# Kernel optimization log

Measured on AMD Instinct MI355X. Metric: run time of the kernel, lower is better.

## Reference

```python
import jax, jax.numpy as jnp
import numpy as np

S, B, C, H = 2048, 2, 512, 8
CC = C // H


def setup_inputs() -> dict:
    key = jax.random.key(0)
    ks = jax.random.split(key, 8)
    x = jax.random.normal(ks[0], (S, B, C), dtype=jnp.float32)
    pe = jax.random.normal(ks[1], (S, B, C), dtype=jnp.float32)
    # strict causal mask: True means masked-out (future positions t > s)
    idx = jnp.arange(S)
    content_mask = (idx[None, :] > idx[:, None])  # (s, t)
    content_mask = jnp.broadcast_to(content_mask[:, :, None], (S, S, B))
    pad = jnp.full((B,), S, dtype=jnp.int64)  # full-length sequences (unused in training path)
    scale = 0.02
    Wqkv = jax.random.normal(ks[2], (3 * C, C), dtype=jnp.float32) * scale
    bqkv = jax.random.normal(ks[3], (3 * C,), dtype=jnp.float32) * scale
    Wc = jax.random.normal(ks[4], (C, C), dtype=jnp.float32) * scale
    bc = jax.random.normal(ks[5], (C,), dtype=jnp.float32) * scale
    return {"x": x, "pe": pe, "content_mask": content_mask, "pad": pad,
            "Wqkv": Wqkv, "bqkv": bqkv, "Wc": Wc, "bc": bc}


def reference(x, pe, content_mask, pad, Wqkv, bqkv, Wc, bc):
    s, b, c = x.shape
    h, cc = H, CC
    qkv = jnp.einsum('sbc,dc->sbd', x + pe, Wqkv) + bqkv  # (s, b, 3c)
    q, k, v = jnp.split(qkv, 3, axis=-1)
    q = q.reshape(s, b, h, cc)
    k = k.reshape(s, b, h, cc)
    v = v.reshape(s, b, h, cc)
    temperature = 1.0 / np.sqrt(cc).astype(np.float32)
    qk = jnp.einsum('sbhc,tbhc->stbh', q, k) * temperature  # (s, t, b, h)
    a = jnp.where(content_mask[:, :, :, None], -jnp.inf, qk)
    p = jax.nn.softmax(a, axis=1)  # softmax over t (dim=1), matching torch
    out = jnp.einsum('stbh,tbhc->sbhc', p, v).reshape(s, b, c)
    out = jnp.einsum('sbc,dc->sbd', out, Wc) + bc
    return out
```

## Files before the change

kernel.cpp:

```cpp
#include <hip/hip_runtime.h>
#include <hip/hip_bf16.h>

#define S_LEN 2048
#define BATCH 2
#define CDIM  512
#define HEADS 8
#define HDIM  64
#define QKVD  1536

typedef float          f32x4  __attribute__((ext_vector_type(4)));
typedef __bf16         bf16x8 __attribute__((ext_vector_type(8)));
typedef unsigned short u16x8  __attribute__((ext_vector_type(8)));

typedef __attribute__((address_space(1))) const unsigned int* gas_ptr;
typedef __attribute__((address_space(3))) unsigned int* las_ptr;

static __device__ __forceinline__ unsigned short f2bf(float x) {
  union { float f; unsigned u; } v; v.f = x;
  unsigned r = v.u + 0x7fffu + ((v.u >> 16) & 1u);
  return (unsigned short)(r >> 16);
}

__global__ void __launch_bounds__(256) prep_kernel(
    const float* __restrict__ x, const float* __restrict__ pe,
    const float* __restrict__ wqkv, const float* __restrict__ wc,
    unsigned short* __restrict__ xpe_bf,
    unsigned short* __restrict__ wqkv_bf,
    unsigned short* __restrict__ wc_bf) {
  const int N1 = S_LEN * BATCH * CDIM;
  const int N2 = QKVD * CDIM;
  const int NP = (N1 + N2 + CDIM * CDIM) / 8;
  const int pkt = blockIdx.x * 256 + threadIdx.x;
  if (pkt >= NP) return;
  int i = pkt * 8;
  u16x8 o;
  if (i < N1) {
    f32x4 a0 = *reinterpret_cast<const f32x4*>(x + i);
    f32x4 a1 = *reinterpret_cast<const f32x4*>(x + i + 4);
    f32x4 b0 = *reinterpret_cast<const f32x4*>(pe + i);
    f32x4 b1 = *reinterpret_cast<const f32x4*>(pe + i + 4);
#pragma unroll
    for (int j = 0; j < 4; ++j) { o[j] = f2bf(a0[j] + b0[j]); o[4 + j] = f2bf(a1[j] + b1[j]); }
    *reinterpret_cast<u16x8*>(xpe_bf + i) = o;
  } else if (i < N1 + N2) {
    i -= N1;
    f32x4 a0 = *reinterpret_cast<const f32x4*>(wqkv + i);
    f32x4 a1 = *reinterpret_cast<const f32x4*>(wqkv + i + 4);
#pragma unroll
    for (int j = 0; j < 4; ++j) { o[j] = f2bf(a0[j]); o[4 + j] = f2bf(a1[j]); }
    *reinterpret_cast<u16x8*>(wqkv_bf + i) = o;
  } else {
    i -= N1 + N2;
    f32x4 a0 = *reinterpret_cast<const f32x4*>(wc + i);
    f32x4 a1 = *reinterpret_cast<const f32x4*>(wc + i + 4);
#pragma unroll
    for (int j = 0; j < 4; ++j) { o[j] = f2bf(a0[j]); o[4 + j] = f2bf(a1[j]); }
    *reinterpret_cast<u16x8*>(wc_bf + i) = o;
  }
}

template <int BM, int BN, int OUT_BF16>
__global__ void __launch_bounds__(256) gemm_lds_kernel(
    const unsigned short* __restrict__ A,
    const unsigned short* __restrict__ Bt,
    const float* __restrict__ bias,
    void* __restrict__ Cout, int M, int N, int K) {
  constexpr int FM = BM / 32;
  constexpr int FN = BN / 32;
  __shared__ unsigned short Alds[BM * 64];
  __shared__ unsigned short Blds[BN * 64];

  const int tid  = threadIdx.x;
  const int w    = tid >> 6;
  const int lane = tid & 63;
  const int wr   = w >> 1, wc = w & 1;
  const int lr   = lane & 15, hi = lane >> 4;
  const int m0   = blockIdx.y * BM;
  const int n0   = blockIdx.x * BN;

  f32x4 acc[FM][FN];
#pragma unroll
  for (int fm = 0; fm < FM; ++fm)
#pragma unroll
    for (int fn = 0; fn < FN; ++fn) acc[fm][fn] = (f32x4){0.f, 0.f, 0.f, 0.f};

  for (int kc = 0; kc < K; kc += 64) {
    __syncthreads();
#pragma unroll
    for (int i = 0; i < BM / 32; ++i) {
      const int idx = tid + i * 256;
      const int row = idx >> 3, col = (idx & 7) * 8;
      const int scol = col ^ ((row & 7) * 8);
      __builtin_amdgcn_global_load_lds(
          (gas_ptr)(const void*)(A + (size_t)(m0 + row) * K + kc + scol),
          (las_ptr)(void*)(Alds + idx * 8), 16, 0, 0);
    }
#pragma unroll
    for (int i = 0; i < BN / 32; ++i) {
      const int idx = tid + i * 256;
      const int row = idx >> 3, col = (idx & 7) * 8;
      const int scol = col ^ ((row & 7) * 8);
      __builtin_amdgcn_global_load_lds(
          (gas_ptr)(const void*)(Bt + (size_t)(n0 + row) * K + kc + scol),
          (las_ptr)(void*)(Blds + idx * 8), 16, 0, 0);
    }
    __syncthreads();

    bf16x8 af[2][FM], bfr[2][FN];
#pragma unroll
    for (int ks = 0; ks < 2; ++ks) {
#pragma unroll
      for (int fm = 0; fm < FM; ++fm) {
        const int row = wr * (BM / 2) + fm * 16 + lr;
        af[ks][fm] = *reinterpret_cast<const bf16x8*>(
            &Alds[row * 64 + ((ks * 32 + hi * 8) ^ ((row & 7) * 8))]);
      }
#pragma unroll
      for (int fn = 0; fn < FN; ++fn) {
        const int row = wc * (BN / 2) + fn * 16 + lr;
        bfr[ks][fn] = *reinterpret_cast<const bf16x8*>(
            &Blds[row * 64 + ((ks * 32 + hi * 8) ^ ((row & 7) * 8))]);
      }
    }
#pragma unroll
    for (int ks = 0; ks < 2; ++ks)
#pragma unroll
      for (int fm = 0; fm < FM; ++fm)
#pragma unroll
        for (int fn = 0; fn < FN; ++fn)
          acc[fm][fn] = __builtin_amdgcn_mfma_f32_16x16x32_bf16(
              af[ks][fm], bfr[ks][fn], acc[fm][fn], 0, 0, 0);
  }

#pragma unroll
  for (int fn = 0; fn < FN; ++fn) {
    const int n = n0 + wc * (BN / 2) + fn * 16 + lr;
    const float bv = bias[n];
#pragma unroll
    for (int fm = 0; fm < FM; ++fm) {
#pragma unroll
      for (int r = 0; r < 4; ++r) {
        const int m = m0 + wr * (BM / 2) + fm * 16 + hi * 4 + r;
        const float val = acc[fm][fn][r] + bv;
        if (OUT_BF16)
          ((unsigned short*)Cout)[(size_t)m * N + n] = f2bf(val);
        else
          ((float*)Cout)[(size_t)m * N + n] = val;
      }
    }
  }
}

#define SCALE_LOG2E 0.18033688011112042f

__device__ __forceinline__ void tile_compute(
    const bf16x8* aq, const bf16x8 kf[4][2], const bf16x8 vf[2][4],
    f32x4* acc, float* rs, unsigned short* Pw,
    int q0, int t0, int lr, int hi) {
  const f32x4 z = (f32x4){0.f, 0.f, 0.f, 0.f};
  f32x4 d[4];
#pragma unroll
  for (int ks = 0; ks < 4; ++ks) {
    f32x4 dd = __builtin_amdgcn_mfma_f32_16x16x32_bf16(aq[0], kf[ks][0], z, 0, 0, 0);
    dd = __builtin_amdgcn_mfma_f32_16x16x32_bf16(aq[1], kf[ks][1], dd, 0, 0, 0);
    d[ks] = dd;
  }
#pragma unroll
  for (int ks = 0; ks < 4; ++ks) {
    const int t = t0 + ks * 16 + lr;
#pragma unroll
    for (int rr = 0; rr < 4; ++rr) {
      const int srow = q0 + hi * 4 + rr;
      float pv = __builtin_exp2f(d[ks][rr] * SCALE_LOG2E);
      pv = (t > srow) ? 0.f : pv;
      d[ks][rr] = pv;
      rs[rr] += pv;
    }
  }
#pragma unroll
  for (int ks = 0; ks < 4; ++ks)
#pragma unroll
    for (int rr = 0; rr < 4; ++rr) {
      const int row = hi * 4 + rr;
      Pw[(row * 64 + ks * 16 + lr) ^ ((row & 7) << 3)] = f2bf(d[ks][rr]);
    }
  bf16x8 pa[2];
#pragma unroll
  for (int kk = 0; kk < 2; ++kk)
    pa[kk] = *reinterpret_cast<const bf16x8*>(
        &Pw[(lr * 64 + kk * 32 + hi * 8) ^ ((lr & 7) << 3)]);
#pragma unroll
  for (int nt = 0; nt < 4; ++nt) {
    acc[nt] = __builtin_amdgcn_mfma_f32_16x16x32_bf16(pa[0], vf[0][nt], acc[nt], 0, 0, 0);
    acc[nt] = __builtin_amdgcn_mfma_f32_16x16x32_bf16(pa[1], vf[1][nt], acc[nt], 0, 0, 0);
  }
}

__global__ void __launch_bounds__(128) attn_kernel(
    const unsigned short* __restrict__ qkv,
    unsigned short* __restrict__ attn_out) {
  __shared__ unsigned short Klds[64 * 64];
  __shared__ unsigned short Vlds[64 * 64];
  __shared__ unsigned short Plds[2][16 * 64];

  const int qb   = blockIdx.x;
  const int h    = blockIdx.y;
  const int b    = blockIdx.z;
  const int tid  = threadIdx.x;
  const int w    = tid >> 6;
  const int lane = tid & 63;
  const int lr   = lane & 15;
  const int hi   = lane >> 4;

  const int p   = qb * 2 + w;
  const int q0A = p * 16;
  const int q0B = (127 - p) * 16;
  const int NT  = ((2047 - 32 * qb) >> 6) + 1;

  const int RS = BATCH * QKVD;
  const unsigned short* Qbase = qkv + (size_t)b * QKVD + h * HDIM;
  const unsigned short* Kbase = Qbase + CDIM;
  const unsigned short* Vbase = Qbase + 2 * CDIM;

  bf16x8 aqA[2], aqB[2];
#pragma unroll
  for (int kk = 0; kk < 2; ++kk) {
    aqA[kk] = *reinterpret_cast<const bf16x8*>(
        Qbase + (size_t)(q0A + lr) * RS + kk * 32 + hi * 8);
    aqB[kk] = *reinterpret_cast<const bf16x8*>(
        Qbase + (size_t)(q0B + lr) * RS + kk * 32 + hi * 8);
  }

  f32x4 accA[4], accB[4];
  float rsA[4], rsB[4];
#pragma unroll
  for (int nt = 0; nt < 4; ++nt) {
    accA[nt] = (f32x4){0.f, 0.f, 0.f, 0.f};
    accB[nt] = (f32x4){0.f, 0.f, 0.f, 0.f};
  }
#pragma unroll
  for (int rr = 0; rr < 4; ++rr) { rsA[rr] = 0.f; rsB[rr] = 0.f; }

  const int kr = tid & 63, khalf = tid >> 6;
  const int va = tid & 31, vq = tid >> 5;
  unsigned short* Pw = Plds[w];

  for (int it = 0; it < NT; ++it) {
    const int t0 = it * 64;
    __syncthreads();
#pragma unroll
    for (int c = 0; c < 4; ++c) {
      const int cc = khalf * 4 + c;
      bf16x8 kv = *reinterpret_cast<const bf16x8*>(
          Kbase + (size_t)(t0 + kr) * RS + cc * 8);
      *reinterpret_cast<bf16x8*>(
          &Klds[(kr * 64 + cc * 8) ^ ((kr & 7) << 3)]) = kv;
    }
#pragma unroll
    for (int c = 0; c < 2; ++c) {
      const int cc = vq * 2 + c;
      const unsigned short* vp = Vbase + (size_t)(t0 + 2 * va) * RS + cc * 8;
      u16x8 v0 = *reinterpret_cast<const u16x8*>(vp);
      u16x8 v1 = *reinterpret_cast<const u16x8*>(vp + RS);
#pragma unroll
      for (int j = 0; j < 8; ++j) {
        const int dim = cc * 8 + j;
        const unsigned val = (unsigned)v0[j] | ((unsigned)v1[j] << 16);
        *reinterpret_cast<unsigned*>(
            &Vlds[(dim * 64 + 2 * va) ^ ((dim & 7) << 3)]) = val;
      }
    }
    __syncthreads();

    bf16x8 kf[4][2], vf[2][4];
#pragma unroll
    for (int ks = 0; ks < 4; ++ks)
#pragma unroll
      for (int kk = 0; kk < 2; ++kk) {
        const int row = ks * 16 + lr;
        kf[ks][kk] = *reinterpret_cast<const bf16x8*>(
            &Klds[(row * 64 + kk * 32 + hi * 8) ^ ((row & 7) << 3)]);
      }
#pragma unroll
    for (int kk = 0; kk < 2; ++kk)
#pragma unroll
      for (int nt = 0; nt < 4; ++nt) {
        const int row = nt * 16 + lr;
        vf[kk][nt] = *reinterpret_cast<const bf16x8*>(
            &Vlds[(row * 64 + kk * 32 + hi * 8) ^ ((row & 7) << 3)]);
      }

    if (t0 <= q0A + 15)
      tile_compute(aqA, kf, vf, accA, rsA, Pw, q0A, t0, lr, hi);
    if (t0 <= q0B + 15)
      tile_compute(aqB, kf, vf, accB, rsB, Pw, q0B, t0, lr, hi);
  }

#pragma unroll
  for (int rr = 0; rr < 4; ++rr) {
    float v = rsA[rr];
    v += __shfl_xor(v, 1); v += __shfl_xor(v, 2);
    v += __shfl_xor(v, 4); v += __shfl_xor(v, 8);
    rsA[rr] = 1.f / v;
    v = rsB[rr];
    v += __shfl_xor(v, 1); v += __shfl_xor(v, 2);
    v += __shfl_xor(v, 4); v += __shfl_xor(v, 8);
    rsB[rr] = 1.f / v;
  }
#pragma unroll
  for (int nt = 0; nt < 4; ++nt)
#pragma unroll
    for (int rr = 0; rr < 4; ++rr) {
      const int c = h * HDIM + nt * 16 + lr;
      const int sA = q0A + hi * 4 + rr;
      attn_out[((size_t)sA * BATCH + b) * CDIM + c] = f2bf(accA[nt][rr] * rsA[rr]);
      const int sB = q0B + hi * 4 + rr;
      attn_out[((size_t)sB * BATCH + b) * CDIM + c] = f2bf(accB[nt][rr] * rsB[rr]);
    }
}

extern "C" void kernel_launch(void* const* d_in, const int* in_sizes, int n_in,
                              void* d_out, int out_size, void* d_ws, size_t ws_size,
                              hipStream_t stream) {
  const float* x    = (const float*)d_in[0];
  const float* pe   = (const float*)d_in[1];
  const float* wqkv = (const float*)d_in[4];
  const float* bqkv = (const float*)d_in[5];
  const float* wc   = (const float*)d_in[6];
  const float* bc   = (const float*)d_in[7];

  unsigned short* xpe_bf  = (unsigned short*)d_ws;
  unsigned short* wqkv_bf = xpe_bf  + (size_t)S_LEN * BATCH * CDIM;
  unsigned short* wc_bf   = wqkv_bf + (size_t)QKVD * CDIM;
  unsigned short* qkv_bf  = wc_bf   + (size_t)CDIM * CDIM;
  unsigned short* attn_bf = qkv_bf  + (size_t)S_LEN * BATCH * QKVD;

  const int NP = (S_LEN * BATCH * CDIM + QKVD * CDIM + CDIM * CDIM) / 8;
  prep_kernel<<<dim3((NP + 255) / 256), dim3(256), 0, stream>>>(
      x, pe, wqkv, wc, xpe_bf, wqkv_bf, wc_bf);
  gemm_lds_kernel<64, 128, 1>
      <<<dim3(QKVD / 128, (S_LEN * BATCH) / 64), dim3(256), 0, stream>>>(
          xpe_bf, wqkv_bf, bqkv, (void*)qkv_bf, S_LEN * BATCH, QKVD, CDIM);
  attn_kernel<<<dim3(32, HEADS, BATCH), dim3(128), 0, stream>>>(qkv_bf, attn_bf);
  gemm_lds_kernel<64, 64, 0>
      <<<dim3(CDIM / 64, (S_LEN * BATCH) / 64), dim3(256), 0, stream>>>(
          attn_bf, wc_bf, bc, d_out, S_LEN * BATCH, CDIM, CDIM);
}
```

Before: 183.3 us.

## Write V transposed from QKV GEMM and stream K/V fragments directly in attention

The QKV GEMM epilogue now writes Q/K into a compact buffer and V transposed per (batch, head) into a separate buffer. The attention kernel drops LDS staging and barriers for K/V and loads MFMA fragments straight from global memory, double-buffered in registers. It also switches to one 16-row query tile per wave with 4 waves per block. Load balance changes: each wave handles one causal tile instead of a paired short/long pair, so work across blocks is uneven. The transposed V stores are scattered 2-byte writes, and K/V reuse across waves now depends on cache instead of LDS.

```diff
diff --git a/kernel.cpp b/kernel.cpp
--- a/kernel.cpp
+++ b/kernel.cpp
@@ -59,12 +59,13 @@
   }
 }
 
-template <int BM, int BN, int OUT_BF16>
+template <int BM, int BN, int MODE>
 __global__ void __launch_bounds__(256) gemm_lds_kernel(
     const unsigned short* __restrict__ A,
     const unsigned short* __restrict__ Bt,
     const float* __restrict__ bias,
-    void* __restrict__ Cout, int M, int N, int K) {
+    void* __restrict__ out0, unsigned short* __restrict__ out1,
+    int M, int N, int K) {
   constexpr int FM = BM / 32;
   constexpr int FN = BN / 32;
   __shared__ unsigned short Alds[BM * 64];
@@ -142,10 +143,17 @@
       for (int r = 0; r < 4; ++r) {
         const int m = m0 + wr * (BM / 2) + fm * 16 + hi * 4 + r;
         const float val = acc[fm][fn][r] + bv;
-        if (OUT_BF16)
-          ((unsigned short*)Cout)[(size_t)m * N + n] = f2bf(val);
-        else
-          ((float*)Cout)[(size_t)m * N + n] = val;
+        if (MODE == 0) {
+          ((float*)out0)[(size_t)m * N + n] = val;
+        } else {
+          if (n0 < 2 * CDIM) {
+            ((unsigned short*)out0)[(size_t)m * (2 * CDIM) + n] = f2bf(val);
+          } else {
+            const int d = n - 2 * CDIM, hh = d >> 6, dim = d & 63;
+            const int s = m >> 1, bb = m & 1;
+            out1[(((size_t)(bb * HEADS + hh)) * HDIM + dim) * S_LEN + s] = f2bf(val);
+          }
+        }
       }
     }
   }
@@ -196,126 +204,87 @@
   }
 }
 
-__global__ void __launch_bounds__(128) attn_kernel(
-    const unsigned short* __restrict__ qkv,
+#define LOADK(dst, t0)                                                      \
+  _Pragma("unroll") for (int ks = 0; ks < 4; ++ks)                          \
+  _Pragma("unroll") for (int kk = 0; kk < 2; ++kk)                          \
+    dst[ks][kk] = *reinterpret_cast<const bf16x8*>(                         \
+        Kb + (size_t)((t0) + ks * 16 + lr) * 2048 + kk * 32 + hi * 8);
+
+#define LOADV(dst, t0)                                                      \
+  _Pragma("unroll") for (int kk = 0; kk < 2; ++kk)                          \
+  _Pragma("unroll") for (int nt = 0; nt < 4; ++nt)                          \
+    dst[kk][nt] = *reinterpret_cast<const bf16x8*>(                         \
+        Vb + (size_t)(nt * 16 + lr) * 2048 + (t0) + kk * 32 + hi * 8);
+
+__global__ void __launch_bounds__(256, 2) attn_kernel(
+    const unsigned short* __restrict__ qk,
+    const unsigned short* __restrict__ vT,
     unsigned short* __restrict__ attn_out) {
-  __shared__ unsigned short Klds[64 * 64];
-  __shared__ unsigned short Vlds[64 * 64];
-  __shared__ unsigned short Plds[2][16 * 64];
-
-  const int qb   = blockIdx.x;
-  const int h    = blockIdx.y;
-  const int b    = blockIdx.z;
+  __shared__ unsigned short Plds[4][2][16 * 64];
   const int tid  = threadIdx.x;
   const int w    = tid >> 6;
   const int lane = tid & 63;
   const int lr   = lane & 15;
   const int hi   = lane >> 4;
-
-  const int p   = qb * 2 + w;
-  const int q0A = p * 16;
-  const int q0B = (127 - p) * 16;
-  const int NT  = ((2047 - 32 * qb) >> 6) + 1;
-
-  const int RS = BATCH * QKVD;
-  const unsigned short* Qbase = qkv + (size_t)b * QKVD + h * HDIM;
-  const unsigned short* Kbase = Qbase + CDIM;
-  const unsigned short* Vbase = Qbase + 2 * CDIM;
-
-  bf16x8 aqA[2], aqB[2];
-#pragma unroll
-  for (int kk = 0; kk < 2; ++kk) {
-    aqA[kk] = *reinterpret_cast<const bf16x8*>(
-        Qbase + (size_t)(q0A + lr) * RS + kk * 32 + hi * 8);
-    aqB[kk] = *reinterpret_cast<const bf16x8*>(
-        Qbase + (size_t)(q0B + lr) * RS + kk * 32 + hi * 8);
-  }
-
-  f32x4 accA[4], accB[4];
-  float rsA[4], rsB[4];
-#pragma unroll
-  for (int nt = 0; nt < 4; ++nt) {
-    accA[nt] = (f32x4){0.f, 0.f, 0.f, 0.f};
-    accB[nt] = (f32x4){0.f, 0.f, 0.f, 0.f};
-  }
-#pragma unroll
-  for (int rr = 0; rr < 4; ++rr) { rsA[rr] = 0.f; rsB[rr] = 0.f; }
-
-  const int kr = tid & 63, khalf = tid >> 6;
-  const int va = tid & 31, vq = tid >> 5;
-  unsigned short* Pw = Plds[w];
-
-  for (int it = 0; it < NT; ++it) {
-    const int t0 = it * 64;
-    __syncthreads();
-#pragma unroll
-    for (int c = 0; c < 4; ++c) {
-      const int cc = khalf * 4 + c;
-      bf16x8 kv = *reinterpret_cast<const bf16x8*>(
-          Kbase + (size_t)(t0 + kr) * RS + cc * 8);
-      *reinterpret_cast<bf16x8*>(
-          &Klds[(kr * 64 + cc * 8) ^ ((kr & 7) << 3)]) = kv;
-    }
-#pragma unroll
-    for (int c = 0; c < 2; ++c) {
-      const int cc = vq * 2 + c;
-      const unsigned short* vp = Vbase + (size_t)(t0 + 2 * va) * RS + cc * 8;
-      u16x8 v0 = *reinterpret_cast<const u16x8*>(vp);
-      u16x8 v1 = *reinterpret_cast<const u16x8*>(vp + RS);
-#pragma unroll
-      for (int j = 0; j < 8; ++j) {
-        const int dim = cc * 8 + j;
-        const unsigned val = (unsigned)v0[j] | ((unsigned)v1[j] << 16);
-        *reinterpret_cast<unsigned*>(
-            &Vlds[(dim * 64 + 2 * va) ^ ((dim & 7) << 3)]) = val;
-      }
-    }
-    __syncthreads();
-
-    bf16x8 kf[4][2], vf[2][4];
-#pragma unroll
-    for (int ks = 0; ks < 4; ++ks)
-#pragma unroll
-      for (int kk = 0; kk < 2; ++kk) {
-        const int row = ks * 16 + lr;
-        kf[ks][kk] = *reinterpret_cast<const bf16x8*>(
-            &Klds[(row * 64 + kk * 32 + hi * 8) ^ ((row & 7) << 3)]);
-      }
-#pragma unroll
-    for (int kk = 0; kk < 2; ++kk)
-#pragma unroll
-      for (int nt = 0; nt < 4; ++nt) {
-        const int row = nt * 16 + lr;
-        vf[kk][nt] = *reinterpret_cast<const bf16x8*>(
-            &Vlds[(row * 64 + kk * 32 + hi * 8) ^ ((row & 7) << 3)]);
-      }
-
-    if (t0 <= q0A + 15)
-      tile_compute(aqA, kf, vf, accA, rsA, Pw, q0A, t0, lr, hi);
-    if (t0 <= q0B + 15)
-      tile_compute(aqB, kf, vf, accB, rsB, Pw, q0B, t0, lr, hi);
-  }
+  const int h    = blockIdx.y;
+  const int b    = blockIdx.z;
+  const int qt   = 127 - (blockIdx.x * 4 + w);
+  const int q0   = qt * 16;
+  const int NT   = (q0 + 15) / 64 + 1;
+
+  const unsigned short* Qb = qk + (size_t)b * 1024 + h * HDIM;
+  const unsigned short* Kb = Qb + CDIM;
+  const unsigned short* Vb = vT + ((size_t)(b * HEADS + h)) * HDIM * S_LEN;
+
+  bf16x8 aq[2];
+#pragma unroll
+  for (int kk = 0; kk < 2; ++kk)
+    aq[kk] = *reinterpret_cast<const bf16x8*>(
+        Qb + (size_t)(q0 + lr) * 2048 + kk * 32 + hi * 8);
+
+  f32x4 acc[4];
+  float rs[4];
+#pragma unroll
+  for (int nt = 0; nt < 4; ++nt) acc[nt] = (f32x4){0.f, 0.f, 0.f, 0.f};
+#pragma unroll
+  for (int rr = 0; rr < 4; ++rr) rs[rr] = 0.f;
+
+  unsigned short* PwA = &Plds[w][0][0];
+  unsigned short* PwB = &Plds[w][1][0];
+
+  bf16x8 kfA[4][2], vfA[2][4], kfB[4][2], vfB[2][4];
+  LOADK(kfA, 0)
+  LOADV(vfA, 0)
+
+  int it = 0;
+  while (it + 1 < NT) {
+    const int tB = (it + 1) * 64;
+    LOADK(kfB, tB)
+    LOADV(vfB, tB)
+    tile_compute(aq, kfA, vfA, acc, rs, PwA, q0, it * 64, lr, hi);
+    const int tA = (it + 2 < NT) ? (it + 2) * 64 : tB;
+    LOADK(kfA, tA)
+    LOADV(vfA, tA)
+    tile_compute(aq, kfB, vfB, acc, rs, PwB, q0, tB, lr, hi);
+    it += 2;
+  }
+  if (it < NT)
+    tile_compute(aq, kfA, vfA, acc, rs, PwA, q0, it * 64, lr, hi);
 
 #pragma unroll
   for (int rr = 0; rr < 4; ++rr) {
-    float v = rsA[rr];
+    float v = rs[rr];
     v += __shfl_xor(v, 1); v += __shfl_xor(v, 2);
     v += __shfl_xor(v, 4); v += __shfl_xor(v, 8);
-    rsA[rr] = 1.f / v;
-    v = rsB[rr];
-    v += __shfl_xor(v, 1); v += __shfl_xor(v, 2);
-    v += __shfl_xor(v, 4); v += __shfl_xor(v, 8);
-    rsB[rr] = 1.f / v;
+    rs[rr] = 1.f / v;
   }
 #pragma unroll
   for (int nt = 0; nt < 4; ++nt)
 #pragma unroll
     for (int rr = 0; rr < 4; ++rr) {
       const int c = h * HDIM + nt * 16 + lr;
-      const int sA = q0A + hi * 4 + rr;
-      attn_out[((size_t)sA * BATCH + b) * CDIM + c] = f2bf(accA[nt][rr] * rsA[rr]);
-      const int sB = q0B + hi * 4 + rr;
-      attn_out[((size_t)sB * BATCH + b) * CDIM + c] = f2bf(accB[nt][rr] * rsB[rr]);
+      const int s = q0 + hi * 4 + rr;
+      attn_out[((size_t)s * BATCH + b) * CDIM + c] = f2bf(acc[nt][rr] * rs[rr]);
     }
 }
 
@@ -332,17 +301,18 @@
   unsigned short* xpe_bf  = (unsigned short*)d_ws;
   unsigned short* wqkv_bf = xpe_bf  + (size_t)S_LEN * BATCH * CDIM;
   unsigned short* wc_bf   = wqkv_bf + (size_t)QKVD * CDIM;
-  unsigned short* qkv_bf  = wc_bf   + (size_t)CDIM * CDIM;
-  unsigned short* attn_bf = qkv_bf  + (size_t)S_LEN * BATCH * QKVD;
+  unsigned short* qk_bf   = wc_bf   + (size_t)CDIM * CDIM;
+  unsigned short* vT_bf   = qk_bf   + (size_t)S_LEN * BATCH * 2 * CDIM;
+  unsigned short* attn_bf = xpe_bf;
 
   const int NP = (S_LEN * BATCH * CDIM + QKVD * CDIM + CDIM * CDIM) / 8;
   prep_kernel<<<dim3((NP + 255) / 256), dim3(256), 0, stream>>>(
       x, pe, wqkv, wc, xpe_bf, wqkv_bf, wc_bf);
-  gemm_lds_kernel<64, 128, 1>
+  gemm_lds_kernel<64, 128, 2>
       <<<dim3(QKVD / 128, (S_LEN * BATCH) / 64), dim3(256), 0, stream>>>(
-          xpe_bf, wqkv_bf, bqkv, (void*)qkv_bf, S_LEN * BATCH, QKVD, CDIM);
-  attn_kernel<<<dim3(32, HEADS, BATCH), dim3(128), 0, stream>>>(qkv_bf, attn_bf);
+          xpe_bf, wqkv_bf, bqkv, (void*)qk_bf, vT_bf, S_LEN * BATCH, QKVD, CDIM);
+  attn_kernel<<<dim3(32, HEADS, BATCH), dim3(256), 0, stream>>>(qk_bf, vT_bf, attn_bf);
   gemm_lds_kernel<64, 64, 0>
       <<<dim3(CDIM / 64, (S_LEN * BATCH) / 64), dim3(256), 0, stream>>>(
-          attn_bf, wc_bf, bc, d_out, S_LEN * BATCH, CDIM, CDIM);
-}
+          attn_bf, wc_bf, bc, d_out, nullptr, S_LEN * BATCH, CDIM, CDIM);
+}
```

New measurement: 237.5 us. +29.6%, slower.

## Split attention key range across two blocks and add a partial-sum reduce kernel

Applied to the files above, without the earlier changes.

Each query-pair block is split into two blocks, each covering half of the key tiles. This doubles the attention grid so more work is in flight on the GPU. Each half writes unnormalised partial outputs in bf16 and its row sums, and a new reduce kernel adds the two halves and normalises them. K tiles are now loaded straight into LDS with global_load_lds instead of going through registers. The cost is an extra kernel launch, extra global traffic for the partials, and some precision loss from rounding the partials to bf16.

```diff
diff --git a/kernel.cpp b/kernel.cpp
--- a/kernel.cpp
+++ b/kernel.cpp
@@ -19,6 +19,10 @@
   union { float f; unsigned u; } v; v.f = x;
   unsigned r = v.u + 0x7fffu + ((v.u >> 16) & 1u);
   return (unsigned short)(r >> 16);
+}
+static __device__ __forceinline__ float bf2f(unsigned short x) {
+  union { unsigned u; float f; } v; v.u = (unsigned)x << 16;
+  return v.f;
 }
 
 __global__ void __launch_bounds__(256) prep_kernel(
@@ -196,14 +200,18 @@
   }
 }
 
-__global__ void __launch_bounds__(128) attn_kernel(
+__global__ void __launch_bounds__(128) attn_part_kernel(
     const unsigned short* __restrict__ qkv,
-    unsigned short* __restrict__ attn_out) {
+    unsigned short* __restrict__ pacc0,
+    unsigned short* __restrict__ pacc1,
+    float* __restrict__ prs) {
   __shared__ unsigned short Klds[64 * 64];
   __shared__ unsigned short Vlds[64 * 64];
   __shared__ unsigned short Plds[2][16 * 64];
 
-  const int qb   = blockIdx.x;
+  const int bx   = blockIdx.x;
+  const int qb   = bx >> 1;
+  const int e    = bx & 1;
   const int h    = blockIdx.y;
   const int b    = blockIdx.z;
   const int tid  = threadIdx.x;
@@ -216,6 +224,9 @@
   const int q0A = p * 16;
   const int q0B = (127 - p) * 16;
   const int NT  = ((2047 - 32 * qb) >> 6) + 1;
+  const int NTh = NT >> 1;
+  const int lo  = e ? NTh : 0;
+  const int hiT = e ? NT : NTh;
 
   const int RS = BATCH * QKVD;
   const unsigned short* Qbase = qkv + (size_t)b * QKVD + h * HDIM;
@@ -241,20 +252,20 @@
 #pragma unroll
   for (int rr = 0; rr < 4; ++rr) { rsA[rr] = 0.f; rsB[rr] = 0.f; }
 
-  const int kr = tid & 63, khalf = tid >> 6;
   const int va = tid & 31, vq = tid >> 5;
   unsigned short* Pw = Plds[w];
 
-  for (int it = 0; it < NT; ++it) {
+  for (int it = lo; it < hiT; ++it) {
     const int t0 = it * 64;
     __syncthreads();
 #pragma unroll
-    for (int c = 0; c < 4; ++c) {
-      const int cc = khalf * 4 + c;
-      bf16x8 kv = *reinterpret_cast<const bf16x8*>(
-          Kbase + (size_t)(t0 + kr) * RS + cc * 8);
-      *reinterpret_cast<bf16x8*>(
-          &Klds[(kr * 64 + cc * 8) ^ ((kr & 7) << 3)]) = kv;
+    for (int i = 0; i < 4; ++i) {
+      const int idx = tid + i * 128;
+      const int row = idx >> 3, col = (idx & 7) * 8;
+      const int scol = col ^ ((row & 7) * 8);
+      __builtin_amdgcn_global_load_lds(
+          (gas_ptr)(const void*)(Kbase + (size_t)(t0 + row) * RS + scol),
+          (las_ptr)(void*)(Klds + idx * 8), 16, 0, 0);
     }
 #pragma unroll
     for (int c = 0; c < 2; ++c) {
@@ -296,16 +307,26 @@
       tile_compute(aqB, kf, vf, accB, rsB, Pw, q0B, t0, lr, hi);
   }
 
+  unsigned short* pacc = e ? pacc1 : pacc0;
 #pragma unroll
   for (int rr = 0; rr < 4; ++rr) {
     float v = rsA[rr];
     v += __shfl_xor(v, 1); v += __shfl_xor(v, 2);
     v += __shfl_xor(v, 4); v += __shfl_xor(v, 8);
-    rsA[rr] = 1.f / v;
+    rsA[rr] = v;
     v = rsB[rr];
     v += __shfl_xor(v, 1); v += __shfl_xor(v, 2);
     v += __shfl_xor(v, 4); v += __shfl_xor(v, 8);
-    rsB[rr] = 1.f / v;
+    rsB[rr] = v;
+  }
+  if (lr == 0) {
+#pragma unroll
+    for (int rr = 0; rr < 4; ++rr) {
+      const int sA = q0A + hi * 4 + rr;
+      const int sB = q0B + hi * 4 + rr;
+      prs[(((size_t)e * S_LEN + sA) * BATCH + b) * HEADS + h] = rsA[rr];
+      prs[(((size_t)e * S_LEN + sB) * BATCH + b) * HEADS + h] = rsB[rr];
+    }
   }
 #pragma unroll
   for (int nt = 0; nt < 4; ++nt)
@@ -313,10 +334,33 @@
     for (int rr = 0; rr < 4; ++rr) {
       const int c = h * HDIM + nt * 16 + lr;
       const int sA = q0A + hi * 4 + rr;
-      attn_out[((size_t)sA * BATCH + b) * CDIM + c] = f2bf(accA[nt][rr] * rsA[rr]);
+      pacc[((size_t)sA * BATCH + b) * CDIM + c] = f2bf(accA[nt][rr]);
       const int sB = q0B + hi * 4 + rr;
-      attn_out[((size_t)sB * BATCH + b) * CDIM + c] = f2bf(accB[nt][rr] * rsB[rr]);
-    }
+      pacc[((size_t)sB * BATCH + b) * CDIM + c] = f2bf(accB[nt][rr]);
+    }
+}
+
+__global__ void __launch_bounds__(256) reduce_kernel(
+    const unsigned short* __restrict__ pacc1,
+    const float* __restrict__ prs,
+    unsigned short* __restrict__ out) {
+  const int t = blockIdx.x * 256 + threadIdx.x;
+  const int i8 = t * 8;
+  const int c = i8 & 511;
+  const int sb = i8 >> 9;
+  const int b = sb & 1;
+  const int s = sb >> 1;
+  const int h = c >> 6;
+  const float r0 = prs[(((size_t)0 * S_LEN + s) * BATCH + b) * HEADS + h];
+  const float r1 = prs[(((size_t)1 * S_LEN + s) * BATCH + b) * HEADS + h];
+  const float inv = 1.f / (r0 + r1);
+  u16x8 a = *reinterpret_cast<const u16x8*>(out + i8);
+  u16x8 bb = *reinterpret_cast<const u16x8*>(pacc1 + i8);
+  u16x8 o;
+#pragma unroll
+  for (int j = 0; j < 8; ++j)
+    o[j] = f2bf((bf2f(a[j]) + bf2f(bb[j])) * inv);
+  *reinterpret_cast<u16x8*>(out + i8) = o;
 }
 
 extern "C" void kernel_launch(void* const* d_in, const int* in_sizes, int n_in,
@@ -334,6 +378,9 @@
   unsigned short* wc_bf   = wqkv_bf + (size_t)QKVD * CDIM;
   unsigned short* qkv_bf  = wc_bf   + (size_t)CDIM * CDIM;
   unsigned short* attn_bf = qkv_bf  + (size_t)S_LEN * BATCH * QKVD;
+  unsigned short* pacc0 = attn_bf;
+  unsigned short* pacc1 = xpe_bf;
+  float*          prs   = (float*)wqkv_bf;
 
   const int NP = (S_LEN * BATCH * CDIM + QKVD * CDIM + CDIM * CDIM) / 8;
   prep_kernel<<<dim3((NP + 255) / 256), dim3(256), 0, stream>>>(
@@ -341,7 +388,10 @@
   gemm_lds_kernel<64, 128, 1>
       <<<dim3(QKVD / 128, (S_LEN * BATCH) / 64), dim3(256), 0, stream>>>(
           xpe_bf, wqkv_bf, bqkv, (void*)qkv_bf, S_LEN * BATCH, QKVD, CDIM);
-  attn_kernel<<<dim3(32, HEADS, BATCH), dim3(128), 0, stream>>>(qkv_bf, attn_bf);
+  attn_part_kernel<<<dim3(64, HEADS, BATCH), dim3(128), 0, stream>>>(
+      qkv_bf, pacc0, pacc1, prs);
+  reduce_kernel<<<dim3(S_LEN * BATCH * CDIM / 8 / 256), dim3(256), 0, stream>>>(
+      pacc1, prs, pacc0);
   gemm_lds_kernel<64, 64, 0>
       <<<dim3(CDIM / 64, (S_LEN * BATCH) / 64), dim3(256), 0, stream>>>(
           attn_bf, wc_bf, bc, d_out, S_LEN * BATCH, CDIM, CDIM);
```

After: 160.5 us. 1.14x faster.
